# Kernel optimization log

Hardware: AMD Instinct MI355X
Metric: run time of the kernel (lower is better)

## Reference

```python
import jax, jax.numpy as jnp
import numpy as np

VOCAB, EMBED, CONV_C, HID, LABELS = 50257, 512, 512, 1024, 128
B, S = 32, 1024

def setup_inputs() -> dict:
    key = jax.random.key(0)
    ks = jax.random.split(key, 8)
    sc = lambda d: 1.0 / np.sqrt(d)
    return {
        "token_ids": jax.random.randint(ks[0], (B, S), 0, VOCAB),
        "emb_table": jax.random.normal(ks[1], (VOCAB, EMBED), jnp.float32) * 0.02,
        "conv_w": jax.random.normal(ks[2], (CONV_C, EMBED), jnp.float32) * sc(EMBED),
        "conv_b": jnp.zeros((CONV_C,), jnp.float32),
        "dec_w1": jax.random.normal(ks[3], (CONV_C, HID), jnp.float32) * sc(CONV_C),
        "dec_b1": jnp.zeros((HID,), jnp.float32),
        "dec_w2": jax.random.normal(ks[4], (HID, LABELS), jnp.float32) * sc(HID),
        "dec_b2": jnp.zeros((LABELS,), jnp.float32),
    }

def reference(token_ids, emb_table, conv_w, conv_b, dec_w1, dec_b1, dec_w2, dec_b2):
    # Embedding lookup: [B, S, E]
    x = emb_table[token_ids]
    # DocNN encoder on a length-1 sequence = kernel-1 conv + relu (+ trivial max-over-time)
    h = jax.nn.relu(jnp.einsum('bse,ce->bsc', x, conv_w) + conv_b)  # [B,S,C]
    # MLP decoder per word
    z = jax.nn.relu(jnp.einsum('bsc,ch->bsh', h, dec_w1) + dec_b1)  # [B,S,H]
    logits = jnp.einsum('bsh,hl->bsl', z, dec_w2) + dec_b2          # [B,S,L]
    # torch.cat over dim 0 of per-word outputs -> flat [B*S, L]
    return logits.reshape(-1, logits.shape[-1])
```

## Files before the change

kernel.cpp:

```cpp
#include <hip/hip_runtime.h>

typedef __bf16 bf16;
typedef __bf16 bf16x4 __attribute__((ext_vector_type(4)));
typedef __bf16 bf16x8 __attribute__((ext_vector_type(8)));
typedef float f32x4 __attribute__((ext_vector_type(4)));

#define NROWS 32768
#define EMBED 512
#define CONV_C 512
#define HID 1024
#define LABELS 128

__device__ inline void async16(const void* g, void* l) {
  __builtin_amdgcn_global_load_lds(
      (const __attribute__((address_space(1))) void*)g,
      (__attribute__((address_space(3))) void*)l, 16, 0, 0);
}

__device__ inline bf16x8 cvt8_sw(const float* row, int o0, int o1) {
  f32x4 lo = *(const f32x4*)(row + o0);
  f32x4 hi = *(const f32x4*)(row + o1);
  bf16x8 r;
  r[0] = (bf16)lo[0]; r[1] = (bf16)lo[1]; r[2] = (bf16)lo[2]; r[3] = (bf16)lo[3];
  r[4] = (bf16)hi[0]; r[5] = (bf16)hi[1]; r[6] = (bf16)hi[2]; r[7] = (bf16)hi[3];
  return r;
}


__global__ void cvt_bf16(const float* __restrict__ in, bf16* __restrict__ out, int n) {
  int i = (blockIdx.x * blockDim.x + threadIdx.x) * 4;
  if (i >= n) return;
  float4 v = *(const float4*)(in + i);
  bf16x4 o;
  o.x = (bf16)v.x; o.y = (bf16)v.y; o.z = (bf16)v.z; o.w = (bf16)v.w;
  *(bf16x4*)(out + i) = o;
}

__global__ void transpose_cvt(const float* __restrict__ in, bf16* __restrict__ out,
                              int K, int N) {
  __shared__ float t[64][65];
  int kb = blockIdx.x * 64, nb = blockIdx.y * 64;
  for (int i = threadIdx.x; i < 4096; i += 256) {
    int r = i >> 6, c = i & 63;
    t[r][c] = in[(size_t)(kb + r) * N + nb + c];
  }
  __syncthreads();
  for (int i = threadIdx.x; i < 4096; i += 256) {
    int r = i >> 6, c = i & 63;
    out[(size_t)(nb + r) * K + kb + c] = (bf16)t[c][r];
  }
}

__global__ __launch_bounds__(256) void gemm1_gather(
    const int* __restrict__ tok, const float* __restrict__ emb,
    const bf16* __restrict__ convw, const float* __restrict__ bias,
    bf16* __restrict__ out, int M, int N, int K) {
  __shared__ __attribute__((aligned(16))) float lAf[128 * 32];
  __shared__ __attribute__((aligned(16))) bf16 lB[128 * 32];
  const int tid = threadIdx.x;
  const int wave = tid >> 6, lane = tid & 63;
  const int m0 = blockIdx.x * 128, n0 = blockIdx.y * 128;
  const int wm = (wave & 1) * 64, wn = (wave >> 1) * 64;
  const int lrow = lane & 15, quad = lane >> 4;
  const int slot0 = wave * 64 + lane;

  int arow[4], acol[4];
#pragma unroll
  for (int c = 0; c < 4; ++c) {
    int s = slot0 + c * 256;
    int r = s >> 3, p = s & 7;
    arow[c] = r;
    acol[c] = (p ^ (r & 7)) * 4;
  }
  int trow[4];
#pragma unroll
  for (int c = 0; c < 4; ++c) trow[c] = tok[m0 + arow[c]];

  const f32x4 zero4 = {0.f, 0.f, 0.f, 0.f};
  f32x4 acc[4][4];
#pragma unroll
  for (int i = 0; i < 4; ++i)
#pragma unroll
    for (int j = 0; j < 4; ++j) acc[i][j] = zero4;

  for (int k0 = 0; k0 < K; k0 += 32) {
#pragma unroll
    for (int c = 0; c < 4; ++c)
      async16(emb + (size_t)trow[c] * EMBED + k0 + acol[c],
              lAf + (size_t)(wave * 64 + c * 256) * 4);
#pragma unroll
    for (int c = 0; c < 2; ++c) {
      int s = slot0 + c * 256;
      int r = s >> 2, cs = s & 3;
      async16(convw + (size_t)(n0 + r) * K + k0 + cs * 8,
              lB + (size_t)(wave * 64 + c * 256) * 8);
    }
    __syncthreads();

    bf16x8 a[4], b[4];
#pragma unroll
    for (int t = 0; t < 4; ++t) {
      int r = wm + t * 16 + lrow, sw = r & 7;
      a[t] = cvt8_sw(lAf + r * 32, ((2 * quad) ^ sw) * 4, ((2 * quad + 1) ^ sw) * 4);
      b[t] = *(const bf16x8*)(lB + (wn + t * 16 + lrow) * 32 + quad * 8);
    }
#pragma unroll
    for (int mi = 0; mi < 4; ++mi)
#pragma unroll
      for (int ni = 0; ni < 4; ++ni)
        acc[mi][ni] =
            __builtin_amdgcn_mfma_f32_16x16x32_bf16(a[mi], b[ni], acc[mi][ni], 0, 0, 0);
    __syncthreads();
  }

#pragma unroll
  for (int mi = 0; mi < 4; ++mi) {
#pragma unroll
    for (int ni = 0; ni < 4; ++ni) {
      int col = n0 + wn + ni * 16 + lrow;
      float bv = bias[col];
#pragma unroll
      for (int r = 0; r < 4; ++r) {
        int row = m0 + wm + mi * 16 + quad * 4 + r;
        float v = acc[mi][ni][r] + bv;
        v = v > 0.f ? v : 0.f;
        out[(size_t)row * N + col] = (bf16)v;
      }
    }
  }
}

template <bool RELU, bool OUTBF>
__global__ __launch_bounds__(256) void gemm_bt(const bf16* __restrict__ A,
                                               const bf16* __restrict__ Bt,
                                               const float* __restrict__ bias,
                                               void* __restrict__ out,
                                               int M, int N, int K) {
  __shared__ __attribute__((aligned(16))) bf16 lA[128 * 32];
  __shared__ __attribute__((aligned(16))) bf16 lB[128 * 32];
  const int tid = threadIdx.x;
  const int wave = tid >> 6, lane = tid & 63;
  const int m0 = blockIdx.x * 128, n0 = blockIdx.y * 128;
  const int wm = (wave & 1) * 64, wn = (wave >> 1) * 64;
  const int lrow = lane & 15, quad = lane >> 4;
  const int slot0 = wave * 64 + lane;

  const f32x4 zero4 = {0.f, 0.f, 0.f, 0.f};
  f32x4 acc[4][4];
#pragma unroll
  for (int i = 0; i < 4; ++i)
#pragma unroll
    for (int j = 0; j < 4; ++j) acc[i][j] = zero4;

  for (int k0 = 0; k0 < K; k0 += 32) {
#pragma unroll
    for (int c = 0; c < 2; ++c) {
      int g = slot0 + c * 256;
      int row = g >> 2, cs = g & 3;
      async16(A + (size_t)(m0 + row) * K + k0 + cs * 8,
              lA + (size_t)(wave * 64 + c * 256) * 8);
      async16(Bt + (size_t)(n0 + row) * K + k0 + cs * 8,
              lB + (size_t)(wave * 64 + c * 256) * 8);
    }
    __syncthreads();

    bf16x8 a[4], b[4];
#pragma unroll
    for (int t = 0; t < 4; ++t) {
      a[t] = *(const bf16x8*)(lA + (wm + t * 16 + lrow) * 32 + quad * 8);
      b[t] = *(const bf16x8*)(lB + (wn + t * 16 + lrow) * 32 + quad * 8);
    }
#pragma unroll
    for (int mi = 0; mi < 4; ++mi)
#pragma unroll
      for (int ni = 0; ni < 4; ++ni)
        acc[mi][ni] =
            __builtin_amdgcn_mfma_f32_16x16x32_bf16(a[mi], b[ni], acc[mi][ni], 0, 0, 0);
    __syncthreads();
  }

#pragma unroll
  for (int mi = 0; mi < 4; ++mi) {
#pragma unroll
    for (int ni = 0; ni < 4; ++ni) {
      int col = n0 + wn + ni * 16 + lrow;
      float bv = bias[col];
#pragma unroll
      for (int r = 0; r < 4; ++r) {
        int row = m0 + wm + mi * 16 + quad * 4 + r;
        float v = acc[mi][ni][r] + bv;
        if (RELU) v = v > 0.f ? v : 0.f;
        if (OUTBF)
          ((bf16*)out)[(size_t)row * N + col] = (bf16)v;
        else
          ((float*)out)[(size_t)row * N + col] = v;
      }
    }
  }
}

__global__ __launch_bounds__(256) void gemm_bt64(const bf16* __restrict__ A,
                                                 const bf16* __restrict__ Bt,
                                                 const float* __restrict__ bias,
                                                 float* __restrict__ out,
                                                 int M, int N, int K) {
  __shared__ __attribute__((aligned(16))) bf16 lA[64 * 32];
  __shared__ __attribute__((aligned(16))) bf16 lB[128 * 32];
  const int tid = threadIdx.x;
  const int wave = tid >> 6, lane = tid & 63;
  const int m0 = blockIdx.x * 64, n0 = 0;
  const int wm = (wave & 1) * 32, wn = (wave >> 1) * 64;
  const int lrow = lane & 15, quad = lane >> 4;
  const int slot0 = wave * 64 + lane;

  const f32x4 zero4 = {0.f, 0.f, 0.f, 0.f};
  f32x4 acc[2][4];
#pragma unroll
  for (int i = 0; i < 2; ++i)
#pragma unroll
    for (int j = 0; j < 4; ++j) acc[i][j] = zero4;

  for (int k0 = 0; k0 < K; k0 += 32) {
    {
      int row = slot0 >> 2, cs = slot0 & 3;
      async16(A + (size_t)(m0 + row) * K + k0 + cs * 8,
              lA + (size_t)(wave * 64) * 8);
    }
#pragma unroll
    for (int c = 0; c < 2; ++c) {
      int g = slot0 + c * 256;
      int row = g >> 2, cs = g & 3;
      async16(Bt + (size_t)(n0 + row) * K + k0 + cs * 8,
              lB + (size_t)(wave * 64 + c * 256) * 8);
    }
    __syncthreads();

    bf16x8 a[2], b[4];
#pragma unroll
    for (int t = 0; t < 2; ++t)
      a[t] = *(const bf16x8*)(lA + (wm + t * 16 + lrow) * 32 + quad * 8);
#pragma unroll
    for (int t = 0; t < 4; ++t)
      b[t] = *(const bf16x8*)(lB + (wn + t * 16 + lrow) * 32 + quad * 8);
#pragma unroll
    for (int mi = 0; mi < 2; ++mi)
#pragma unroll
      for (int ni = 0; ni < 4; ++ni)
        acc[mi][ni] =
            __builtin_amdgcn_mfma_f32_16x16x32_bf16(a[mi], b[ni], acc[mi][ni], 0, 0, 0);
    __syncthreads();
  }

#pragma unroll
  for (int mi = 0; mi < 2; ++mi) {
#pragma unroll
    for (int ni = 0; ni < 4; ++ni) {
      int col = n0 + wn + ni * 16 + lrow;
      float bv = bias[col];
#pragma unroll
      for (int r = 0; r < 4; ++r) {
        int row = m0 + wm + mi * 16 + quad * 4 + r;
        out[(size_t)row * N + col] = acc[mi][ni][r] + bv;
      }
    }
  }
}


extern "C" void kernel_launch(void* const* d_in, const int* in_sizes, int n_in,
                              void* d_out, int out_size, void* d_ws, size_t ws_size,
                              hipStream_t stream) {
  const int* tok = (const int*)d_in[0];
  const float* emb = (const float*)d_in[1];
  const float* conv_w = (const float*)d_in[2];
  const float* conv_b = (const float*)d_in[3];
  const float* w1 = (const float*)d_in[4];
  const float* b1 = (const float*)d_in[5];
  const float* w2 = (const float*)d_in[6];
  const float* b2 = (const float*)d_in[7];
  float* out = (float*)d_out;

  char* ws = (char*)d_ws;
  bf16* wtc = (bf16*)(ws);
  bf16* wt1 = (bf16*)(ws + (1u << 19));
  bf16* wt2 = (bf16*)(ws + 3 * (1u << 19));
  bf16* h = (bf16*)(ws + (2u << 20));
  bf16* z = (bf16*)(ws + (34u << 20));

  hipLaunchKernelGGL(cvt_bf16, dim3(256), dim3(256), 0, stream,
                     conv_w, wtc, CONV_C * EMBED);
  hipLaunchKernelGGL(transpose_cvt, dim3(8, 16), dim3(256), 0, stream,
                     w1, wt1, CONV_C, HID);
  hipLaunchKernelGGL(transpose_cvt, dim3(16, 2), dim3(256), 0, stream,
                     w2, wt2, HID, LABELS);

  hipLaunchKernelGGL(gemm1_gather, dim3(NROWS / 128, CONV_C / 128), dim3(256),
                     0, stream, tok, emb, wtc, conv_b, h, NROWS, CONV_C, EMBED);
  hipLaunchKernelGGL((gemm_bt<true, true>), dim3(NROWS / 128, HID / 128), dim3(256),
                     0, stream, h, wt1, b1, (void*)z, NROWS, HID, CONV_C);
  hipLaunchKernelGGL(gemm_bt64, dim3(NROWS / 64, 1), dim3(256),
                     0, stream, z, wt2, b2, out, NROWS, LABELS, HID);
}
```

Baseline: 270.3 us.

## Fuse decoder GEMMs keeping hidden activations in LDS and remap gather-GEMM blocks per XCD

Merges the second and third GEMMs into one kernel. Each 64-row block computes the hidden activations in 128-column chunks, applies bias and ReLU into a swizzled LDS buffer, and accumulates the label projection from that buffer. This removes the 64MB bf16 round trip of z through global memory and one launch. The cost is about 56KB of LDS per block, which lowers occupancy. Separately, the gather GEMM now uses a 1D grid remapped so that the four N-tiles sharing an M-tile run on the same XCD, which is meant to improve L2 reuse of the gathered embedding rows.

```diff
diff --git a/kernel.cpp b/kernel.cpp
--- a/kernel.cpp
+++ b/kernel.cpp
@@ -59,7 +59,10 @@
   __shared__ __attribute__((aligned(16))) bf16 lB[128 * 32];
   const int tid = threadIdx.x;
   const int wave = tid >> 6, lane = tid & 63;
-  const int m0 = blockIdx.x * 128, n0 = blockIdx.y * 128;
+  const int id = blockIdx.x;
+  const int xcd = id & 7, q = id >> 3;
+  const int nb = q & 3, mb = (q >> 2) * 8 + xcd;
+  const int m0 = mb * 128, n0 = nb * 128;
   const int wm = (wave & 1) * 64, wn = (wave >> 1) * 64;
   const int lrow = lane & 15, quad = lane >> 4;
   const int slot0 = wave * 64 + lane;
@@ -130,124 +133,117 @@
   }
 }
 
-template <bool RELU, bool OUTBF>
-__global__ __launch_bounds__(256) void gemm_bt(const bf16* __restrict__ A,
-                                               const bf16* __restrict__ Bt,
-                                               const float* __restrict__ bias,
-                                               void* __restrict__ out,
-                                               int M, int N, int K) {
-  __shared__ __attribute__((aligned(16))) bf16 lA[128 * 32];
-  __shared__ __attribute__((aligned(16))) bf16 lB[128 * 32];
-  const int tid = threadIdx.x;
-  const int wave = tid >> 6, lane = tid & 63;
-  const int m0 = blockIdx.x * 128, n0 = blockIdx.y * 128;
-  const int wm = (wave & 1) * 64, wn = (wave >> 1) * 64;
-  const int lrow = lane & 15, quad = lane >> 4;
-  const int slot0 = wave * 64 + lane;
-
-  const f32x4 zero4 = {0.f, 0.f, 0.f, 0.f};
-  f32x4 acc[4][4];
-#pragma unroll
-  for (int i = 0; i < 4; ++i)
-#pragma unroll
-    for (int j = 0; j < 4; ++j) acc[i][j] = zero4;
-
-  for (int k0 = 0; k0 < K; k0 += 32) {
-#pragma unroll
-    for (int c = 0; c < 2; ++c) {
-      int g = slot0 + c * 256;
-      int row = g >> 2, cs = g & 3;
-      async16(A + (size_t)(m0 + row) * K + k0 + cs * 8,
-              lA + (size_t)(wave * 64 + c * 256) * 8);
-      async16(Bt + (size_t)(n0 + row) * K + k0 + cs * 8,
-              lB + (size_t)(wave * 64 + c * 256) * 8);
-    }
-    __syncthreads();
-
-    bf16x8 a[4], b[4];
-#pragma unroll
-    for (int t = 0; t < 4; ++t) {
-      a[t] = *(const bf16x8*)(lA + (wm + t * 16 + lrow) * 32 + quad * 8);
-      b[t] = *(const bf16x8*)(lB + (wn + t * 16 + lrow) * 32 + quad * 8);
-    }
-#pragma unroll
-    for (int mi = 0; mi < 4; ++mi)
-#pragma unroll
-      for (int ni = 0; ni < 4; ++ni)
-        acc[mi][ni] =
-            __builtin_amdgcn_mfma_f32_16x16x32_bf16(a[mi], b[ni], acc[mi][ni], 0, 0, 0);
-    __syncthreads();
-  }
-
-#pragma unroll
-  for (int mi = 0; mi < 4; ++mi) {
-#pragma unroll
-    for (int ni = 0; ni < 4; ++ni) {
-      int col = n0 + wn + ni * 16 + lrow;
-      float bv = bias[col];
-#pragma unroll
-      for (int r = 0; r < 4; ++r) {
-        int row = m0 + wm + mi * 16 + quad * 4 + r;
-        float v = acc[mi][ni][r] + bv;
-        if (RELU) v = v > 0.f ? v : 0.f;
-        if (OUTBF)
-          ((bf16*)out)[(size_t)row * N + col] = (bf16)v;
-        else
-          ((float*)out)[(size_t)row * N + col] = v;
-      }
-    }
-  }
-}
-
-__global__ __launch_bounds__(256) void gemm_bt64(const bf16* __restrict__ A,
-                                                 const bf16* __restrict__ Bt,
-                                                 const float* __restrict__ bias,
-                                                 float* __restrict__ out,
-                                                 int M, int N, int K) {
+__global__ __launch_bounds__(256) void gemm23_fused(
+    const bf16* __restrict__ h,
+    const bf16* __restrict__ w1t,
+    const bf16* __restrict__ w2t,
+    const float* __restrict__ b1, const float* __restrict__ b2,
+    float* __restrict__ out) {
   __shared__ __attribute__((aligned(16))) bf16 lA[64 * 32];
   __shared__ __attribute__((aligned(16))) bf16 lB[128 * 32];
-  const int tid = threadIdx.x;
-  const int wave = tid >> 6, lane = tid & 63;
-  const int m0 = blockIdx.x * 64, n0 = 0;
+  __shared__ __attribute__((aligned(16))) bf16 zbuf[64 * 128];
+  __shared__ __attribute__((aligned(16))) bf16 lB3[128 * 128];
+  const int tid = threadIdx.x, wave = tid >> 6, lane = tid & 63;
+  const int m0 = blockIdx.x * 64;
   const int wm = (wave & 1) * 32, wn = (wave >> 1) * 64;
   const int lrow = lane & 15, quad = lane >> 4;
   const int slot0 = wave * 64 + lane;
 
   const f32x4 zero4 = {0.f, 0.f, 0.f, 0.f};
-  f32x4 acc[2][4];
+  f32x4 out_acc[2][4];
 #pragma unroll
   for (int i = 0; i < 2; ++i)
 #pragma unroll
-    for (int j = 0; j < 4; ++j) acc[i][j] = zero4;
-
-  for (int k0 = 0; k0 < K; k0 += 32) {
-    {
-      int row = slot0 >> 2, cs = slot0 & 3;
-      async16(A + (size_t)(m0 + row) * K + k0 + cs * 8,
-              lA + (size_t)(wave * 64) * 8);
-    }
-#pragma unroll
-    for (int c = 0; c < 2; ++c) {
-      int g = slot0 + c * 256;
-      int row = g >> 2, cs = g & 3;
-      async16(Bt + (size_t)(n0 + row) * K + k0 + cs * 8,
-              lB + (size_t)(wave * 64 + c * 256) * 8);
-    }
-    __syncthreads();
-
-    bf16x8 a[2], b[4];
-#pragma unroll
-    for (int t = 0; t < 2; ++t)
-      a[t] = *(const bf16x8*)(lA + (wm + t * 16 + lrow) * 32 + quad * 8);
-#pragma unroll
-    for (int t = 0; t < 4; ++t)
-      b[t] = *(const bf16x8*)(lB + (wn + t * 16 + lrow) * 32 + quad * 8);
-#pragma unroll
-    for (int mi = 0; mi < 2; ++mi)
-#pragma unroll
-      for (int ni = 0; ni < 4; ++ni)
-        acc[mi][ni] =
-            __builtin_amdgcn_mfma_f32_16x16x32_bf16(a[mi], b[ni], acc[mi][ni], 0, 0, 0);
+    for (int j = 0; j < 4; ++j) out_acc[i][j] = zero4;
+
+  for (int chunk = 0; chunk < 8; ++chunk) {
+    f32x4 z_acc[2][4];
+#pragma unroll
+    for (int i = 0; i < 2; ++i)
+#pragma unroll
+      for (int j = 0; j < 4; ++j) z_acc[i][j] = zero4;
+
+    const bf16* wB = w1t + (size_t)(chunk * 128) * 512;
+    for (int k0 = 0; k0 < 512; k0 += 32) {
+      {
+        int r = slot0 >> 2, cs = slot0 & 3;
+        async16(h + (size_t)(m0 + r) * 512 + k0 + cs * 8,
+                lA + (size_t)(wave * 64) * 8);
+      }
+#pragma unroll
+      for (int c = 0; c < 2; ++c) {
+        int g = slot0 + c * 256;
+        int r = g >> 2, cs = g & 3;
+        async16(wB + (size_t)r * 512 + k0 + cs * 8,
+                lB + (size_t)(wave * 64 + c * 256) * 8);
+      }
+      __syncthreads();
+
+      bf16x8 a[2], b[4];
+#pragma unroll
+      for (int t = 0; t < 2; ++t)
+        a[t] = *(const bf16x8*)(lA + (wm + t * 16 + lrow) * 32 + quad * 8);
+#pragma unroll
+      for (int t = 0; t < 4; ++t)
+        b[t] = *(const bf16x8*)(lB + (wn + t * 16 + lrow) * 32 + quad * 8);
+#pragma unroll
+      for (int mi = 0; mi < 2; ++mi)
+#pragma unroll
+        for (int ni = 0; ni < 4; ++ni)
+          z_acc[mi][ni] =
+              __builtin_amdgcn_mfma_f32_16x16x32_bf16(a[mi], b[ni], z_acc[mi][ni], 0, 0, 0);
+      __syncthreads();
+    }
+
+#pragma unroll
+    for (int c = 0; c < 8; ++c) {
+      int s = slot0 + c * 256;
+      int r = s >> 4, p = s & 15;
+      int qs = p ^ (r & 7);
+      async16(w2t + (size_t)r * HID + chunk * 128 + qs * 8,
+              lB3 + (size_t)(wave * 64 + c * 256) * 8);
+    }
+#pragma unroll
+    for (int mi = 0; mi < 2; ++mi) {
+#pragma unroll
+      for (int ni = 0; ni < 4; ++ni) {
+        int col = wn + ni * 16 + lrow;
+        float bv = b1[chunk * 128 + col];
+#pragma unroll
+        for (int r = 0; r < 4; ++r) {
+          int row = wm + mi * 16 + quad * 4 + r;
+          float v = z_acc[mi][ni][r] + bv;
+          v = v > 0.f ? v : 0.f;
+          int g = col >> 3, wd = col & 7;
+          int pos = g ^ (row & 7);
+          zbuf[row * 128 + pos * 8 + wd] = (bf16)v;
+        }
+      }
+    }
+    __syncthreads();
+
+#pragma unroll
+    for (int ks = 0; ks < 4; ++ks) {
+      bf16x8 a3[2], b3[4];
+#pragma unroll
+      for (int mi = 0; mi < 2; ++mi) {
+        int row = wm + mi * 16 + lrow;
+        int p = (ks * 4 + quad) ^ (row & 7);
+        a3[mi] = *(const bf16x8*)(zbuf + row * 128 + p * 8);
+      }
+#pragma unroll
+      for (int ni = 0; ni < 4; ++ni) {
+        int row = wn + ni * 16 + lrow;
+        int p = (ks * 4 + quad) ^ (row & 7);
+        b3[ni] = *(const bf16x8*)(lB3 + row * 128 + p * 8);
+      }
+#pragma unroll
+      for (int mi = 0; mi < 2; ++mi)
+#pragma unroll
+        for (int ni = 0; ni < 4; ++ni)
+          out_acc[mi][ni] =
+              __builtin_amdgcn_mfma_f32_16x16x32_bf16(a3[mi], b3[ni], out_acc[mi][ni], 0, 0, 0);
+    }
     __syncthreads();
   }
 
@@ -255,12 +251,12 @@
   for (int mi = 0; mi < 2; ++mi) {
 #pragma unroll
     for (int ni = 0; ni < 4; ++ni) {
-      int col = n0 + wn + ni * 16 + lrow;
-      float bv = bias[col];
+      int col = wn + ni * 16 + lrow;
+      float bv = b2[col];
 #pragma unroll
       for (int r = 0; r < 4; ++r) {
         int row = m0 + wm + mi * 16 + quad * 4 + r;
-        out[(size_t)row * N + col] = acc[mi][ni][r] + bv;
+        out[(size_t)row * LABELS + col] = out_acc[mi][ni][r] + bv;
       }
     }
   }
@@ -285,7 +281,6 @@
   bf16* wt1 = (bf16*)(ws + (1u << 19));
   bf16* wt2 = (bf16*)(ws + 3 * (1u << 19));
   bf16* h = (bf16*)(ws + (2u << 20));
-  bf16* z = (bf16*)(ws + (34u << 20));
 
   hipLaunchKernelGGL(cvt_bf16, dim3(256), dim3(256), 0, stream,
                      conv_w, wtc, CONV_C * EMBED);
@@ -294,10 +289,8 @@
   hipLaunchKernelGGL(transpose_cvt, dim3(16, 2), dim3(256), 0, stream,
                      w2, wt2, HID, LABELS);
 
-  hipLaunchKernelGGL(gemm1_gather, dim3(NROWS / 128, CONV_C / 128), dim3(256),
+  hipLaunchKernelGGL(gemm1_gather, dim3(1024), dim3(256),
                      0, stream, tok, emb, wtc, conv_b, h, NROWS, CONV_C, EMBED);
-  hipLaunchKernelGGL((gemm_bt<true, true>), dim3(NROWS / 128, HID / 128), dim3(256),
-                     0, stream, h, wt1, b1, (void*)z, NROWS, HID, CONV_C);
-  hipLaunchKernelGGL(gemm_bt64, dim3(NROWS / 64, 1), dim3(256),
-                     0, stream, z, wt2, b2, out, NROWS, LABELS, HID);
-}
+  hipLaunchKernelGGL(gemm23_fused, dim3(NROWS / 64), dim3(256),
+                     0, stream, h, wt1, wt2, b1, b2, out);
+}
```

New measurement: 289.1 us. +6.9%, slower.
